# Optimization experiments

Measured on AMD Instinct MI355X. Metric: run time of the kernel, lower is better.

Reference implementation:

```python
import jax, jax.numpy as jnp
import numpy as np

B, N, C, H = 16, 1024, 768, 12
HD = C // H
SCALE = HD ** -0.5


def setup_inputs() -> dict:
    key = jax.random.key(0)
    k1, k2, k3 = jax.random.split(key, 3)
    x = jax.random.normal(k1, (B, N, C), dtype=jnp.float32)
    W_qkv = jax.random.normal(k2, (C, 3 * C), dtype=jnp.float32) * (C ** -0.5)
    W_proj = jax.random.normal(k3, (C, C), dtype=jnp.float32) * (C ** -0.5)
    b_proj = jnp.zeros((C,), dtype=jnp.float32)
    return {"x": x, "W_qkv": W_qkv, "W_proj": W_proj, "b_proj": b_proj}


def reference(x, W_qkv, W_proj, b_proj):
    # qkv projection: [B, N, 3C] -> chunk into q, k, v
    qkv = x @ W_qkv
    q, k, v = jnp.split(qkv, 3, axis=-1)
    # reshape to [B, H, N, HD]
    q = q.reshape(B, N, H, HD).transpose(0, 2, 1, 3)
    k = k.reshape(B, N, H, HD).transpose(0, 2, 1, 3)
    v = v.reshape(B, N, H, HD).transpose(0, 2, 1, 3)
    # manual attention: scores, softmax, weighted sum
    attn = jnp.einsum("bhqd,bhkd->bhqk", q, k) * SCALE
    attn = jax.nn.softmax(attn, axis=-1)
    out = jnp.einsum("bhqk,bhkd->bhqd", attn, v)
    out = out.transpose(0, 2, 1, 3).reshape(B, N, C)
    # output projection
    return out @ W_proj + b_proj
```

## Files before the change

### kernel.cpp

```cpp
#include <hip/hip_runtime.h>

#define B_   16
#define NH   12
#define SEQ  1024
#define CD   768
#define HD_  64
#define MTOT (B_ * SEQ)
#define QSCALE 0.18033688f

typedef __attribute__((ext_vector_type(4)))  float  f32x4;
typedef __attribute__((ext_vector_type(16))) float  f32x16;
typedef __attribute__((ext_vector_type(8)))  __bf16 bf16x8;
typedef __attribute__((ext_vector_type(2)))  unsigned u32x2;

#define WAITV4  asm volatile("s_waitcnt vmcnt(4)" ::: "memory")
#define WAITV0  asm volatile("s_waitcnt vmcnt(0)" ::: "memory")
#define LGKM0   asm volatile("s_waitcnt lgkmcnt(0)" ::: "memory")
#define BAR     __builtin_amdgcn_s_barrier()
#define SB0     __builtin_amdgcn_sched_barrier(0)

__device__ __forceinline__ unsigned short f2bf(float f) {
  unsigned u = __float_as_uint(f);
  u = (u + 0x7FFFu + ((u >> 16) & 1u)) >> 16;
  return (unsigned short)u;
}

__device__ __forceinline__ void gload16(const void* g, void* l) {
  __builtin_amdgcn_global_load_lds(
      (const __attribute__((address_space(1))) void*)g,
      (__attribute__((address_space(3))) void*)l, 16, 0, 0);
}

__device__ __forceinline__ u32x2 pswap(unsigned x, unsigned y) {
  return __builtin_amdgcn_permlane32_swap(x, y, false, false);
}


__global__ __launch_bounds__(256)
void prep_kernel(const float* __restrict__ x,
                 const float* __restrict__ Wqkv,
                 const float* __restrict__ Wproj,
                 unsigned short* __restrict__ xb,
                 unsigned short* __restrict__ wqT,
                 unsigned short* __restrict__ wpT) {
  __shared__ float tile[32][33];
  const int bid = blockIdx.x;
  const int tid = threadIdx.x;
  if (bid < 12288) {
    const int i = bid * 256 + tid;
    float4 f = reinterpret_cast<const float4*>(x)[i];
    uint2 o;
    o.x = (unsigned)f2bf(f.x) | ((unsigned)f2bf(f.y) << 16);
    o.y = (unsigned)f2bf(f.z) | ((unsigned)f2bf(f.w) << 16);
    reinterpret_cast<uint2*>(xb)[i] = o;
  } else {
    const float* W;
    unsigned short* Wt;
    int N, b2;
    if (bid < 12288 + 1728) { b2 = bid - 12288; W = Wqkv; Wt = wqT; N = 2304; }
    else                    { b2 = bid - 14016; W = Wproj; Wt = wpT; N = 768; }
    const int nb = N / 32;
    const int j0 = (b2 % nb) * 32, k0 = (b2 / nb) * 32;
    const int tx = tid & 31, ty = tid >> 5;
    #pragma unroll
    for (int i = 0; i < 4; i++)
      tile[ty + 8 * i][tx] = W[(size_t)(k0 + ty + 8 * i) * N + j0 + tx];
    __syncthreads();
    #pragma unroll
    for (int i = 0; i < 4; i++)
      Wt[(size_t)(j0 + ty + 8 * i) * 768 + k0 + tx] = f2bf(tile[tx][ty + 8 * i]);
  }
}


__device__ __forceinline__ bf16x8 ldsA64(const unsigned short* buf, int row, int g) {
  int byte = (row << 6) + ((g << 4) ^ (((row >> 1) & 3) << 4));
  return *reinterpret_cast<const bf16x8*>((const char*)buf + byte);
}
__device__ __forceinline__ bf16x8 lds128(const unsigned short* buf, int row, int cb) {
  int byte = (row << 7) + (cb ^ ((row & 7) << 4));
  return *reinterpret_cast<const bf16x8*>((const char*)buf + byte);
}


template <int MODE>
__global__ __launch_bounds__(256, 3)
void gemm128_kernel(const unsigned short* __restrict__ A,
                    const unsigned short* __restrict__ Bt,
                    unsigned short* __restrict__ qkvOut,
                    unsigned short* __restrict__ vtOut,
                    float* __restrict__ outF,
                    const float* __restrict__ bias) {
  constexpr int K = 768;
  __shared__ unsigned short sbuf[24576];
  unsigned short* const A0 = sbuf;
  unsigned short* const Bb0 = sbuf + 4096;
  unsigned short* const A1 = sbuf + 8192;
  unsigned short* const Bb1 = sbuf + 12288;
  unsigned short* const A2 = sbuf + 16384;
  unsigned short* const Bb2 = sbuf + 20480;

  const int tid = threadIdx.x;
  const int lane = tid & 63;
  const int wave = tid >> 6;
  const int wm = (wave >> 1) << 6;
  const int wn = (wave & 1) << 6;
  const int m0 = blockIdx.x << 7;
  const int j0 = blockIdx.y << 7;

  const int sr = tid >> 2;
  const int sc = (tid & 3) << 4;
  const int scs = sc ^ (((sr >> 1) & 3) << 4);

  f32x4 acc[4][4] = {};

  const char* const ab  = (const char*)(A  + (size_t)(m0 + sr) * K) + scs;
  const char* const ab2 = (const char*)(A  + (size_t)(m0 + sr + 64) * K) + scs;
  const char* const bb  = (const char*)(Bt + (size_t)(j0 + sr) * K) + scs;
  const char* const bb2 = (const char*)(Bt + (size_t)(j0 + sr + 64) * K) + scs;

  auto stageT = [&](int kt, unsigned short* Ad, unsigned short* Bd) {
    const int kb = kt * 64;
    gload16(ab  + kb, (char*)Ad + tid * 16);
    gload16(ab2 + kb, (char*)Ad + 4096 + tid * 16);
    gload16(bb  + kb, (char*)Bd + tid * 16);
    gload16(bb2 + kb, (char*)Bd + 4096 + tid * 16);
  };

  auto computeT = [&](const unsigned short* As, const unsigned short* Bs) {
    bf16x8 af[4], bf[4];
    const int g = lane >> 4;
    #pragma unroll
    for (int fr = 0; fr < 4; fr++) af[fr] = ldsA64(As, wm + fr * 16 + (lane & 15), g);
    #pragma unroll
    for (int fn = 0; fn < 4; fn++) bf[fn] = ldsA64(Bs, wn + fn * 16 + (lane & 15), g);
    __builtin_amdgcn_s_setprio(1);
    #pragma unroll
    for (int fr = 0; fr < 4; fr++)
      #pragma unroll
      for (int fn = 0; fn < 4; fn++)
        acc[fr][fn] = __builtin_amdgcn_mfma_f32_16x16x32_bf16(af[fr], bf[fn],
                                                              acc[fr][fn], 0, 0, 0);
    __builtin_amdgcn_s_setprio(0);
  };

  stageT(0, A0, Bb0);
  stageT(1, A1, Bb1);

  #pragma unroll 1
  for (int t = 0; t < 21; t += 3) {
    WAITV4; BAR; SB0;
    stageT(t + 2, A2, Bb2);
    computeT(A0, Bb0);

    WAITV4; BAR; SB0;
    stageT(t + 3, A0, Bb0);
    computeT(A1, Bb1);

    WAITV4; BAR; SB0;
    stageT(t + 4, A1, Bb1);
    computeT(A2, Bb2);
  }
  WAITV4; BAR; SB0;
  stageT(23, A2, Bb2);
  computeT(A0, Bb0);
  WAITV4; BAR; SB0;
  computeT(A1, Bb1);
  WAITV0; BAR; SB0;
  computeT(A2, Bb2);

  const int g4 = (lane >> 4) << 2;

  if (MODE == 0) {
    LGKM0; BAR;
    const bool secV = (j0 >= 1536);
    const float scale = (j0 < 768) ? QSCALE : 1.0f;
    char* const ct = (char*)sbuf;
    #pragma unroll
    for (int fr = 0; fr < 4; fr++) {
      #pragma unroll
      for (int fn = 0; fn < 4; fn++) {
        const int j_l = wn + fn * 16 + (lane & 15);
        const int m_l = wm + fr * 16 + g4;
        #pragma unroll
        for (int r = 0; r < 4; r++) {
          const unsigned short v = f2bf(acc[fr][fn][r] * scale);
          const int addr = secV ? (j_l * 288 + (m_l + r) * 2)
                                : ((m_l + r) * 288 + j_l * 2);
          *reinterpret_cast<unsigned short*>(ct + addr) = v;
        }
      }
    }
    LGKM0; BAR;
    const int c = tid & 15, r0 = tid >> 4;
    if (!secV) {
      char* const gb = (char*)qkvOut + (size_t)m0 * 4608 + j0 * 2 + c * 16;
      #pragma unroll
      for (int k = 0; k < 8; k++) {
        const int row = r0 + 16 * k;
        const uint4 d = *reinterpret_cast<const uint4*>(ct + row * 288 + c * 16);
        *reinterpret_cast<uint4*>(gb + (size_t)row * 4608) = d;
      }
    } else {
      const int b = m0 >> 10, nblk = (m0 & 1023) >> 7;
      const int h0 = (j0 - 1536) >> 6;
      char* const vb = (char*)vtOut +
          ((size_t)(b * NH + h0) * 65536 + (size_t)nblk * 8192) * 2 + c * 16;
      #pragma unroll
      for (int k = 0; k < 8; k++) {
        const int row = r0 + 16 * k;
        const uint4 d = *reinterpret_cast<const uint4*>(ct + row * 288 + c * 16);
        const size_t off = ((size_t)(row >> 6) * 65536 + (size_t)(row & 63) * 128) * 2;
        *reinterpret_cast<uint4*>(vb + off) = d;
      }
    }
  } else {
    #pragma unroll
    for (int fr = 0; fr < 4; fr++) {
      #pragma unroll
      for (int fn = 0; fn < 4; fn++) {
        const int jl = j0 + wn + fn * 16 + (lane & 15);
        const int mb = m0 + wm + fr * 16 + g4;
        const float bv = bias[jl];
        #pragma unroll
        for (int r = 0; r < 4; r++)
          outF[(size_t)(mb + r) * CD + jl] = acc[fr][fn][r] + bv;
      }
    }
  }
}


__global__ __launch_bounds__(256, 4)
void attn_kernel(const unsigned short* __restrict__ qkvB,
                 const unsigned short* __restrict__ Vt,
                 unsigned short* __restrict__ Og) {
  __shared__ unsigned short ldsbuf[16384];
  __shared__ float sStat[2][4][32];

  unsigned short* const K0 = ldsbuf;
  unsigned short* const V0 = ldsbuf + 4096;
  unsigned short* const K1 = ldsbuf + 8192;
  unsigned short* const V1 = ldsbuf + 12288;
  unsigned short* const Qs = ldsbuf + 8192;

  const int tid = threadIdx.x;
  const int lane = tid & 63;
  const int wave = tid >> 6;
  const int half = lane >> 5;
  const int q_l = lane & 31;
  const int bh = blockIdx.x;
  const int q0 = blockIdx.y * 128;
  const int b = bh / NH, head = bh - b * NH;

  const int sr = tid >> 3;
  const int scs = ((tid & 7) << 4) ^ ((sr & 7) << 4);

  const char* const xb_ = (const char*)qkvB + (size_t)b * 1024 * 4608;
  const int qoff = head * 128;
  const int koff = qoff + 1536;
  const char* const vb0 = (const char*)Vt + (size_t)bh * 131072;

  {
    #pragma unroll
    for (int i = 0; i < 4; i++)
      gload16(xb_ + (size_t)(q0 + sr + 32 * i) * 4608 + qoff + scs,
              (char*)Qs + (tid + 256 * i) * 16);
    gload16(xb_ + (size_t)sr * 4608 + koff + scs, (char*)K0 + tid * 16);
    gload16(xb_ + (size_t)(sr + 32) * 4608 + koff + scs, (char*)K0 + 4096 + tid * 16);
    gload16(vb0 + sr * 256 + scs, (char*)V0 + tid * 16);
    gload16(vb0 + (sr + 32) * 256 + scs, (char*)V0 + 4096 + tid * 16);
  }
  __syncthreads();

  bf16x8 qf[4];
  #pragma unroll
  for (int c = 0; c < 4; c++)
    qf[c] = lds128(Qs, wave * 32 + q_l, 32 * c + 16 * half);
  __syncthreads();

  f32x16 o0 = {}, o1 = {};
  float mrun = -1e30f, lrun = 0.f;

  for (int t = 0; t < 16; t++) {
    const unsigned short* const Kc = (t & 1) ? K1 : K0;
    const unsigned short* const Vc = (t & 1) ? V1 : V0;
    unsigned short* const Kn = (t & 1) ? K0 : K1;
    unsigned short* const Vn = (t & 1) ? V0 : V1;
    if (t < 15) {
      const int kv1 = (t + 1) * 64;
      const char* const vtile = vb0 + (kv1 >> 7) * 16384 + ((kv1 >> 6) & 1) * 128;
      gload16(xb_ + (size_t)(kv1 + sr) * 4608 + koff + scs, (char*)Kn + tid * 16);
      gload16(xb_ + (size_t)(kv1 + sr + 32) * 4608 + koff + scs,
              (char*)Kn + 4096 + tid * 16);
      gload16(vtile + sr * 256 + scs, (char*)Vn + tid * 16);
      gload16(vtile + (sr + 32) * 256 + scs, (char*)Vn + 4096 + tid * 16);
    }

    f32x16 s0 = {}, s1 = {};
    #pragma unroll
    for (int c = 0; c < 4; c++) {
      bf16x8 kf0 = lds128(Kc, q_l, 32 * c + 16 * half);
      bf16x8 kf1 = lds128(Kc, 32 + q_l, 32 * c + 16 * half);
      s0 = __builtin_amdgcn_mfma_f32_32x32x16_bf16(kf0, qf[c], s0, 0, 0, 0);
      s1 = __builtin_amdgcn_mfma_f32_32x32x16_bf16(kf1, qf[c], s1, 0, 0, 0);
    }

    float vmax = fmaxf(s0[0], s1[0]);
    #pragma unroll
    for (int r = 1; r < 16; r++) vmax = fmaxf(vmax, fmaxf(s0[r], s1[r]));
    {
      u32x2 mx = pswap(__float_as_uint(vmax), __float_as_uint(vmax));
      vmax = fmaxf(__uint_as_float(mx[0]), __uint_as_float(mx[1]));
    }

    if (!__all(vmax <= mrun + 8.0f)) {
      const float mnew = fmaxf(mrun, vmax);
      const float corr = __builtin_amdgcn_exp2f(mrun - mnew);
      mrun = mnew;
      lrun *= corr;
      if (lane < 32) sStat[0][wave][q_l] = corr;
      f32x4 c4[4];
      #pragma unroll
      for (int j = 0; j < 4; j++)
        c4[j] = *reinterpret_cast<const f32x4*>(&sStat[0][wave][4 * half + 8 * j]);
      #pragma unroll
      for (int r = 0; r < 16; r++) {
        const float cc = c4[r >> 2][r & 3];
        o0[r] *= cc;
        o1[r] *= cc;
      }
    }

    float tsum = 0.f;
    #pragma unroll
    for (int r = 0; r < 16; r++) {
      const float p0 = __builtin_amdgcn_exp2f(s0[r] - mrun);
      const float p1 = __builtin_amdgcn_exp2f(s1[r] - mrun);
      s0[r] = p0; s1[r] = p1;
      tsum += p0 + p1;
    }
    {
      u32x2 ts = pswap(__float_as_uint(tsum), __float_as_uint(tsum));
      tsum = __uint_as_float(ts[0]) + __uint_as_float(ts[1]);
    }
    lrun += tsum;

    unsigned pk[2][8];
    #pragma unroll
    for (int w = 0; w < 8; w++) {
      asm("v_cvt_pk_bf16_f32 %0, %1, %2"
          : "=v"(pk[0][w]) : "v"(s0[2 * w]), "v"(s0[2 * w + 1]));
      asm("v_cvt_pk_bf16_f32 %0, %1, %2"
          : "=v"(pk[1][w]) : "v"(s1[2 * w]), "v"(s1[2 * w + 1]));
    }

    #pragma unroll
    for (int c = 0; c < 4; c++) {
      const int st = c >> 1, cc = c & 1;
      u32x2 rA = pswap(pk[st][4 * cc + 0], pk[st][4 * cc + 2]);
      u32x2 rB = pswap(pk[st][4 * cc + 1], pk[st][4 * cc + 3]);
      union { unsigned u[4]; bf16x8 v; } pa;
      pa.u[0] = rA[0]; pa.u[1] = rB[0]; pa.u[2] = rA[1]; pa.u[3] = rB[1];
      bf16x8 vf0 = lds128(Vc, q_l, 32 * c + 16 * half);
      bf16x8 vf1 = lds128(Vc, 32 + q_l, 32 * c + 16 * half);
      o0 = __builtin_amdgcn_mfma_f32_32x32x16_bf16(pa.v, vf0, o0, 0, 0, 0);
      o1 = __builtin_amdgcn_mfma_f32_32x32x16_bf16(pa.v, vf1, o1, 0, 0, 0);
    }
    __syncthreads();
  }

  if (lane < 32) sStat[1][wave][q_l] = lrun;
  f32x4 rl4[4];
  #pragma unroll
  for (int j = 0; j < 4; j++) {
    f32x4 lv = *reinterpret_cast<const f32x4*>(&sStat[1][wave][4 * half + 8 * j]);
    #pragma unroll
    for (int e = 0; e < 4; e++) rl4[j][e] = __builtin_amdgcn_rcpf(lv[e]);
  }
  #pragma unroll
  for (int r = 0; r < 16; r++) {
    const int qq = q0 + wave * 32 + (r & 3) + 8 * (r >> 2) + 4 * half;
    const float rl = rl4[r >> 2][r & 3];
    const size_t base = ((size_t)b * SEQ + qq) * CD + head * HD_;
    Og[base + q_l]      = f2bf(o0[r] * rl);
    Og[base + 32 + q_l] = f2bf(o1[r] * rl);
  }
}


extern "C" void kernel_launch(void* const* d_in, const int* in_sizes, int n_in,
                              void* d_out, int out_size, void* d_ws, size_t ws_size,
                              hipStream_t stream) {
  const float* x     = (const float*)d_in[0];
  const float* Wqkv  = (const float*)d_in[1];
  const float* Wproj = (const float*)d_in[2];
  const float* bproj = (const float*)d_in[3];

  char* ws = (char*)d_ws;
  unsigned short* qkvB = (unsigned short*)(ws + 0);
  unsigned short* Vt   = (unsigned short*)(ws + 75497472);
  unsigned short* xb   = (unsigned short*)(ws + 100663296);
  unsigned short* ao   = (unsigned short*)(ws + 100663296);
  unsigned short* wqT  = (unsigned short*)(ws + 125829120);
  unsigned short* wpT  = (unsigned short*)(ws + 129368064);
  if (ws_size < 130547712ull) return;

  prep_kernel<<<14592, 256, 0, stream>>>(x, Wqkv, Wproj, xb, wqT, wpT);
  gemm128_kernel<0><<<dim3(128, 18), 256, 0, stream>>>(xb, wqT, qkvB, Vt,
                                                       nullptr, nullptr);
  attn_kernel<<<dim3(B_ * NH, SEQ / 128), 256, 0, stream>>>(qkvB, Vt, ao);
  gemm128_kernel<1><<<dim3(128, 6), 256, 0, stream>>>(ao, wpT, nullptr, nullptr,
                                                      (float*)d_out, bproj);
}
```

Before: 195.3 us.

## Split GEMM into QKV and proj kernels with tuned pipelines and coalesced epilogue

Splits the templated GEMM into two specialized kernels. The QKV GEMM moves from triple to double buffering with less LDS and a 296-byte padded transpose stride, so four blocks can fit per CU instead of three. The output projection now stages fp32 accumulators through LDS in two halves and writes bias-added rows as coalesced float4 stores, replacing scattered scalar stores. Double buffering adds an extra barrier per K step, which may expose more load latency.

```diff
diff --git a/kernel.cpp b/kernel.cpp
--- a/kernel.cpp
+++ b/kernel.cpp
@@ -83,14 +83,141 @@
 }
 
 
-template <int MODE>
+__global__ __launch_bounds__(256, 4)
+void gemm_qkv_kernel(const unsigned short* __restrict__ A,
+                     const unsigned short* __restrict__ Bt,
+                     unsigned short* __restrict__ qkvOut,
+                     unsigned short* __restrict__ vtOut) {
+  constexpr int K = 768;
+  __shared__ unsigned short sbuf[18944];
+  unsigned short* const A0 = sbuf;
+  unsigned short* const Bb0 = sbuf + 4096;
+  unsigned short* const A1 = sbuf + 8192;
+  unsigned short* const Bb1 = sbuf + 12288;
+
+  const int tid = threadIdx.x;
+  const int lane = tid & 63;
+  const int wave = tid >> 6;
+  const int wm = (wave >> 1) << 6;
+  const int wn = (wave & 1) << 6;
+  const int m0 = blockIdx.x << 7;
+  const int j0 = blockIdx.y << 7;
+
+  const int sr = tid >> 2;
+  const int sc = (tid & 3) << 4;
+  const int scs = sc ^ (((sr >> 1) & 3) << 4);
+
+  f32x4 acc[4][4] = {};
+
+  const char* const ab  = (const char*)(A  + (size_t)(m0 + sr) * K) + scs;
+  const char* const ab2 = (const char*)(A  + (size_t)(m0 + sr + 64) * K) + scs;
+  const char* const bb  = (const char*)(Bt + (size_t)(j0 + sr) * K) + scs;
+  const char* const bb2 = (const char*)(Bt + (size_t)(j0 + sr + 64) * K) + scs;
+
+  auto stageT = [&](int kt, unsigned short* Ad, unsigned short* Bd) {
+    const int kb = kt * 64;
+    gload16(ab  + kb, (char*)Ad + tid * 16);
+    gload16(ab2 + kb, (char*)Ad + 4096 + tid * 16);
+    gload16(bb  + kb, (char*)Bd + tid * 16);
+    gload16(bb2 + kb, (char*)Bd + 4096 + tid * 16);
+  };
+
+  auto computeT = [&](const unsigned short* As, const unsigned short* Bs) {
+    bf16x8 af[4], bf[4];
+    const int g = lane >> 4;
+    #pragma unroll
+    for (int fr = 0; fr < 4; fr++) af[fr] = ldsA64(As, wm + fr * 16 + (lane & 15), g);
+    #pragma unroll
+    for (int fn = 0; fn < 4; fn++) bf[fn] = ldsA64(Bs, wn + fn * 16 + (lane & 15), g);
+    __builtin_amdgcn_s_setprio(1);
+    #pragma unroll
+    for (int fr = 0; fr < 4; fr++)
+      #pragma unroll
+      for (int fn = 0; fn < 4; fn++)
+        acc[fr][fn] = __builtin_amdgcn_mfma_f32_16x16x32_bf16(af[fr], bf[fn],
+                                                              acc[fr][fn], 0, 0, 0);
+    __builtin_amdgcn_s_setprio(0);
+  };
+
+  stageT(0, A0, Bb0);
+  stageT(1, A1, Bb1);
+
+  #pragma unroll 1
+  for (int t = 0; t < 20; t += 2) {
+    WAITV4; BAR; SB0;
+    computeT(A0, Bb0);
+    SB0; LGKM0; BAR;
+    stageT(t + 2, A0, Bb0);
+
+    WAITV4; BAR; SB0;
+    computeT(A1, Bb1);
+    SB0; LGKM0; BAR;
+    stageT(t + 3, A1, Bb1);
+  }
+  WAITV4; BAR; SB0;
+  computeT(A0, Bb0);
+  SB0; LGKM0; BAR;
+  stageT(22, A0, Bb0);
+  WAITV4; BAR; SB0;
+  computeT(A1, Bb1);
+  SB0; LGKM0; BAR;
+  stageT(23, A1, Bb1);
+  WAITV4; BAR; SB0;
+  computeT(A0, Bb0);
+  WAITV0; BAR; SB0;
+  computeT(A1, Bb1);
+
+  const int g4 = (lane >> 4) << 2;
+  LGKM0; BAR;
+  const bool secV = (j0 >= 1536);
+  const float scale = (j0 < 768) ? QSCALE : 1.0f;
+  char* const ct = (char*)sbuf;
+  #pragma unroll
+  for (int fr = 0; fr < 4; fr++) {
+    #pragma unroll
+    for (int fn = 0; fn < 4; fn++) {
+      const int j_l = wn + fn * 16 + (lane & 15);
+      const int m_l = wm + fr * 16 + g4;
+      #pragma unroll
+      for (int r = 0; r < 4; r++) {
+        const unsigned short v = f2bf(acc[fr][fn][r] * scale);
+        const int addr = secV ? (j_l * 296 + (m_l + r) * 2)
+                              : ((m_l + r) * 296 + j_l * 2);
+        *reinterpret_cast<unsigned short*>(ct + addr) = v;
+      }
+    }
+  }
+  LGKM0; BAR;
+  const int c = tid & 15, r0 = tid >> 4;
+  if (!secV) {
+    char* const gb = (char*)qkvOut + (size_t)m0 * 4608 + j0 * 2 + c * 16;
+    #pragma unroll
+    for (int k = 0; k < 8; k++) {
+      const int row = r0 + 16 * k;
+      const uint4 d = *reinterpret_cast<const uint4*>(ct + row * 296 + c * 16);
+      *reinterpret_cast<uint4*>(gb + (size_t)row * 4608) = d;
+    }
+  } else {
+    const int b = m0 >> 10, nblk = (m0 & 1023) >> 7;
+    const int h0 = (j0 - 1536) >> 6;
+    char* const vb = (char*)vtOut +
+        ((size_t)(b * NH + h0) * 65536 + (size_t)nblk * 8192) * 2 + c * 16;
+    #pragma unroll
+    for (int k = 0; k < 8; k++) {
+      const int row = r0 + 16 * k;
+      const uint4 d = *reinterpret_cast<const uint4*>(ct + row * 296 + c * 16);
+      const size_t off = ((size_t)(row >> 6) * 65536 + (size_t)(row & 63) * 128) * 2;
+      *reinterpret_cast<uint4*>(vb + off) = d;
+    }
+  }
+}
+
+
 __global__ __launch_bounds__(256, 3)
-void gemm128_kernel(const unsigned short* __restrict__ A,
-                    const unsigned short* __restrict__ Bt,
-                    unsigned short* __restrict__ qkvOut,
-                    unsigned short* __restrict__ vtOut,
-                    float* __restrict__ outF,
-                    const float* __restrict__ bias) {
+void gemm_proj_kernel(const unsigned short* __restrict__ A,
+                      const unsigned short* __restrict__ Bt,
+                      float* __restrict__ outF,
+                      const float* __restrict__ bias) {
   constexpr int K = 768;
   __shared__ unsigned short sbuf[24576];
   unsigned short* const A0 = sbuf;
@@ -170,62 +297,31 @@
   computeT(A2, Bb2);
 
   const int g4 = (lane >> 4) << 2;
-
-  if (MODE == 0) {
+  float* const ctf = (float*)sbuf;
+  const int c = tid & 31, rb = tid >> 5;
+  const float4 bv4 = *reinterpret_cast<const float4*>(bias + j0 + c * 4);
+  #pragma unroll
+  for (int p = 0; p < 2; p++) {
     LGKM0; BAR;
-    const bool secV = (j0 >= 1536);
-    const float scale = (j0 < 768) ? QSCALE : 1.0f;
-    char* const ct = (char*)sbuf;
-    #pragma unroll
-    for (int fr = 0; fr < 4; fr++) {
+    if ((wave >> 1) == p) {
       #pragma unroll
-      for (int fn = 0; fn < 4; fn++) {
-        const int j_l = wn + fn * 16 + (lane & 15);
-        const int m_l = wm + fr * 16 + g4;
+      for (int fr = 0; fr < 4; fr++)
         #pragma unroll
-        for (int r = 0; r < 4; r++) {
-          const unsigned short v = f2bf(acc[fr][fn][r] * scale);
-          const int addr = secV ? (j_l * 288 + (m_l + r) * 2)
-                                : ((m_l + r) * 288 + j_l * 2);
-          *reinterpret_cast<unsigned short*>(ct + addr) = v;
+        for (int fn = 0; fn < 4; fn++) {
+          const int col = wn + fn * 16 + (lane & 15);
+          const int lr = fr * 16 + g4;
+          #pragma unroll
+          for (int r = 0; r < 4; r++)
+            ctf[(lr + r) * 132 + col] = acc[fr][fn][r];
         }
-      }
     }
     LGKM0; BAR;
-    const int c = tid & 15, r0 = tid >> 4;
-    if (!secV) {
-      char* const gb = (char*)qkvOut + (size_t)m0 * 4608 + j0 * 2 + c * 16;
-      #pragma unroll
-      for (int k = 0; k < 8; k++) {
-        const int row = r0 + 16 * k;
-        const uint4 d = *reinterpret_cast<const uint4*>(ct + row * 288 + c * 16);
-        *reinterpret_cast<uint4*>(gb + (size_t)row * 4608) = d;
-      }
-    } else {
-      const int b = m0 >> 10, nblk = (m0 & 1023) >> 7;
-      const int h0 = (j0 - 1536) >> 6;
-      char* const vb = (char*)vtOut +
-          ((size_t)(b * NH + h0) * 65536 + (size_t)nblk * 8192) * 2 + c * 16;
-      #pragma unroll
-      for (int k = 0; k < 8; k++) {
-        const int row = r0 + 16 * k;
-        const uint4 d = *reinterpret_cast<const uint4*>(ct + row * 288 + c * 16);
-        const size_t off = ((size_t)(row >> 6) * 65536 + (size_t)(row & 63) * 128) * 2;
-        *reinterpret_cast<uint4*>(vb + off) = d;
-      }
-    }
-  } else {
-    #pragma unroll
-    for (int fr = 0; fr < 4; fr++) {
-      #pragma unroll
-      for (int fn = 0; fn < 4; fn++) {
-        const int jl = j0 + wn + fn * 16 + (lane & 15);
-        const int mb = m0 + wm + fr * 16 + g4;
-        const float bv = bias[jl];
-        #pragma unroll
-        for (int r = 0; r < 4; r++)
-          outF[(size_t)(mb + r) * CD + jl] = acc[fr][fn][r] + bv;
-      }
+    #pragma unroll
+    for (int k = 0; k < 8; k++) {
+      const int row = rb + 8 * k;
+      f32x4 v = *reinterpret_cast<const f32x4*>(&ctf[row * 132 + c * 4]);
+      v[0] += bv4.x; v[1] += bv4.y; v[2] += bv4.z; v[3] += bv4.w;
+      *reinterpret_cast<f32x4*>(outF + (size_t)(m0 + p * 64 + row) * CD + j0 + c * 4) = v;
     }
   }
 }
@@ -407,9 +503,7 @@
   if (ws_size < 130547712ull) return;
 
   prep_kernel<<<14592, 256, 0, stream>>>(x, Wqkv, Wproj, xb, wqT, wpT);
-  gemm128_kernel<0><<<dim3(128, 18), 256, 0, stream>>>(xb, wqT, qkvB, Vt,
-                                                       nullptr, nullptr);
+  gemm_qkv_kernel<<<dim3(128, 18), 256, 0, stream>>>(xb, wqT, qkvB, Vt);
   attn_kernel<<<dim3(B_ * NH, SEQ / 128), 256, 0, stream>>>(qkvB, Vt, ao);
-  gemm128_kernel<1><<<dim3(128, 6), 256, 0, stream>>>(ao, wpT, nullptr, nullptr,
-                                                      (float*)d_out, bproj);
-}
+  gemm_proj_kernel<<<dim3(128, 6), 256, 0, stream>>>(ao, wpT, (float*)d_out, bproj);
+}
```

Measured after the change: 198.4 us. About the same (+1.6%).

## Replace 128x128 GEMM with 256x256 tile, 8-wave, K=128 double-buffered pipeline

Applied to the files above, without the earlier changes.

Rewrites both projection GEMMs to use 256x256 output tiles with 512 threads (8 waves), K-steps of 128, and a double-buffered LDS schedule that interleaves half-tile loads with four MFMA quadrants. The goal is more operand reuse per byte loaded and fewer global loads per FLOP. The output-projection epilogue now goes through LDS for coalesced float4 stores with bias. The grids become small: 576 blocks for QKV and only 192 for the output projection, which can leave many of the 256 CUs idle. The 128 KB LDS footprint also limits occupancy.

```diff
diff --git a/kernel.cpp b/kernel.cpp
--- a/kernel.cpp
+++ b/kernel.cpp
@@ -73,158 +73,204 @@
 }
 
 
-__device__ __forceinline__ bf16x8 ldsA64(const unsigned short* buf, int row, int g) {
-  int byte = (row << 6) + ((g << 4) ^ (((row >> 1) & 3) << 4));
-  return *reinterpret_cast<const bf16x8*>((const char*)buf + byte);
-}
 __device__ __forceinline__ bf16x8 lds128(const unsigned short* buf, int row, int cb) {
   int byte = (row << 7) + (cb ^ ((row & 7) << 4));
   return *reinterpret_cast<const bf16x8*>((const char*)buf + byte);
 }
 
 
+#define READ_AF(FRH)                                                          \
+  _Pragma("unroll") for (int kk = 0; kk < 2; kk++)                            \
+  _Pragma("unroll") for (int i = 0; i < 4; i++)                               \
+    af[kk][i] = lds128(Ac, wm * 128 + (FRH) * 64 + i * 16 + rl, kk * 64 + fcb);
+#define READ_BF(FNH)                                                          \
+  _Pragma("unroll") for (int kk = 0; kk < 2; kk++)                            \
+  _Pragma("unroll") for (int j = 0; j < 2; j++)                               \
+    bf[kk][(FNH) * 2 + j] =                                                   \
+        lds128(Bc, wn * 64 + (FNH) * 32 + j * 16 + rl, kk * 64 + fcb);
+#define MFMA16(FRH, FNH)                                                      \
+  __builtin_amdgcn_s_setprio(1);                                              \
+  _Pragma("unroll") for (int kk = 0; kk < 2; kk++)                            \
+  _Pragma("unroll") for (int i = 0; i < 4; i++)                               \
+  _Pragma("unroll") for (int j = 0; j < 2; j++)                               \
+    acc[(FRH) * 4 + i][(FNH) * 2 + j] = __builtin_amdgcn_mfma_f32_16x16x32_bf16( \
+        af[kk][i], bf[kk][(FNH) * 2 + j], acc[(FRH) * 4 + i][(FNH) * 2 + j],  \
+        0, 0, 0);                                                             \
+  __builtin_amdgcn_s_setprio(0);
+
 template <int MODE>
-__global__ __launch_bounds__(256, 3)
-void gemm128_kernel(const unsigned short* __restrict__ A,
+__global__ __launch_bounds__(512, 2)
+void gemm256_kernel(const unsigned short* __restrict__ A,
                     const unsigned short* __restrict__ Bt,
                     unsigned short* __restrict__ qkvOut,
                     unsigned short* __restrict__ vtOut,
                     float* __restrict__ outF,
                     const float* __restrict__ bias) {
-  constexpr int K = 768;
-  __shared__ unsigned short sbuf[24576];
-  unsigned short* const A0 = sbuf;
-  unsigned short* const Bb0 = sbuf + 4096;
-  unsigned short* const A1 = sbuf + 8192;
-  unsigned short* const Bb1 = sbuf + 12288;
-  unsigned short* const A2 = sbuf + 16384;
-  unsigned short* const Bb2 = sbuf + 20480;
+  __shared__ unsigned short lds[65536];
 
   const int tid = threadIdx.x;
   const int lane = tid & 63;
   const int wave = tid >> 6;
-  const int wm = (wave >> 1) << 6;
-  const int wn = (wave & 1) << 6;
-  const int m0 = blockIdx.x << 7;
-  const int j0 = blockIdx.y << 7;
-
-  const int sr = tid >> 2;
-  const int sc = (tid & 3) << 4;
-  const int scs = sc ^ (((sr >> 1) & 3) << 4);
-
-  f32x4 acc[4][4] = {};
-
-  const char* const ab  = (const char*)(A  + (size_t)(m0 + sr) * K) + scs;
-  const char* const ab2 = (const char*)(A  + (size_t)(m0 + sr + 64) * K) + scs;
-  const char* const bb  = (const char*)(Bt + (size_t)(j0 + sr) * K) + scs;
-  const char* const bb2 = (const char*)(Bt + (size_t)(j0 + sr + 64) * K) + scs;
-
-  auto stageT = [&](int kt, unsigned short* Ad, unsigned short* Bd) {
-    const int kb = kt * 64;
-    gload16(ab  + kb, (char*)Ad + tid * 16);
-    gload16(ab2 + kb, (char*)Ad + 4096 + tid * 16);
-    gload16(bb  + kb, (char*)Bd + tid * 16);
-    gload16(bb2 + kb, (char*)Bd + 4096 + tid * 16);
+  const int wm = wave >> 2;
+  const int wn = wave & 3;
+  const int m0 = blockIdx.x << 8;
+  const int j0 = blockIdx.y << 8;
+  const int rl = lane & 15;
+  const int fcb = (lane >> 4) << 4;
+
+  const int srow = tid >> 3;
+  const int sc16 = (tid & 7) << 4;
+  const int scs = sc16 ^ ((srow & 7) << 4);
+
+  const char* const aRow = (const char*)A  + ((size_t)(m0 + srow) * 768) * 2 + scs;
+  const char* const bRow = (const char*)Bt + ((size_t)(j0 + srow) * 768) * 2 + scs;
+  char* const dRowA = (char*)lds + srow * 128 + sc16;
+
+  f32x4 acc[8][4] = {};
+
+  auto stageA = [&](int kt, int h, int bb) {
+    const char* src = aRow + (size_t)h * 196608 + kt * 128;
+    char* dst = dRowA + bb * 65536 + h * 16384;
+    gload16(src, dst);
+    gload16(src + 98304, dst + 8192);
   };
-
-  auto computeT = [&](const unsigned short* As, const unsigned short* Bs) {
-    bf16x8 af[4], bf[4];
-    const int g = lane >> 4;
-    #pragma unroll
-    for (int fr = 0; fr < 4; fr++) af[fr] = ldsA64(As, wm + fr * 16 + (lane & 15), g);
-    #pragma unroll
-    for (int fn = 0; fn < 4; fn++) bf[fn] = ldsA64(Bs, wn + fn * 16 + (lane & 15), g);
-    __builtin_amdgcn_s_setprio(1);
-    #pragma unroll
-    for (int fr = 0; fr < 4; fr++)
-      #pragma unroll
-      for (int fn = 0; fn < 4; fn++)
-        acc[fr][fn] = __builtin_amdgcn_mfma_f32_16x16x32_bf16(af[fr], bf[fn],
-                                                              acc[fr][fn], 0, 0, 0);
-    __builtin_amdgcn_s_setprio(0);
+  auto stageB = [&](int kt, int h, int bb) {
+    const char* src = bRow + (size_t)h * 196608 + kt * 128;
+    char* dst = dRowA + 32768 + bb * 65536 + h * 16384;
+    gload16(src, dst);
+    gload16(src + 98304, dst + 8192);
   };
 
-  stageT(0, A0, Bb0);
-  stageT(1, A1, Bb1);
+  stageA(0, 0, 0); stageA(0, 1, 0);
+  stageB(0, 0, 0); stageB(0, 1, 0);
+  stageA(1, 0, 1); stageA(1, 1, 1);
+  WAITV4; BAR; SB0;
+
+  bf16x8 af[2][4], bf[2][4];
 
   #pragma unroll 1
-  for (int t = 0; t < 21; t += 3) {
-    WAITV4; BAR; SB0;
-    stageT(t + 2, A2, Bb2);
-    computeT(A0, Bb0);
-
-    WAITV4; BAR; SB0;
-    stageT(t + 3, A0, Bb0);
-    computeT(A1, Bb1);
-
-    WAITV4; BAR; SB0;
-    stageT(t + 4, A1, Bb1);
-    computeT(A2, Bb2);
-  }
-  WAITV4; BAR; SB0;
-  stageT(23, A2, Bb2);
-  computeT(A0, Bb0);
-  WAITV4; BAR; SB0;
-  computeT(A1, Bb1);
-  WAITV0; BAR; SB0;
-  computeT(A2, Bb2);
+  for (int t = 0; t < 12; ++t) {
+    const unsigned short* Ac = lds + (t & 1) * 32768;
+    const unsigned short* Bc = Ac + 16384;
+    const int n = (t & 1) ^ 1;
+    READ_AF(0); READ_BF(0);
+    if (t <= 10) stageB(t + 1, 0, n);
+    BAR; LGKM0; SB0;
+    MFMA16(0, 0);
+    BAR;
+    READ_BF(1);
+    if (t <= 10) stageB(t + 1, 1, n);
+    BAR; LGKM0; SB0;
+    MFMA16(0, 1);
+    BAR;
+    READ_AF(1);
+    if (t <= 9) stageA(t + 2, 0, t & 1);
+    BAR; LGKM0; SB0;
+    MFMA16(1, 1);
+    BAR;
+    if (t <= 9) stageA(t + 2, 1, t & 1);
+    BAR; SB0;
+    MFMA16(1, 0);
+    if (t <= 9) { WAITV4; }
+    else if (t == 10) { WAITV0; }
+    BAR; SB0;
+  }
 
   const int g4 = (lane >> 4) << 2;
 
   if (MODE == 0) {
-    LGKM0; BAR;
     const bool secV = (j0 >= 1536);
     const float scale = (j0 < 768) ? QSCALE : 1.0f;
-    char* const ct = (char*)sbuf;
-    #pragma unroll
-    for (int fr = 0; fr < 4; fr++) {
+    char* const ct = (char*)lds;
+    if (!secV) {
       #pragma unroll
-      for (int fn = 0; fn < 4; fn++) {
-        const int j_l = wn + fn * 16 + (lane & 15);
-        const int m_l = wm + fr * 16 + g4;
+      for (int p = 0; p < 2; p++) {
+        BAR;
+        if (wm == p) {
+          #pragma unroll
+          for (int fr = 0; fr < 8; fr++)
+            #pragma unroll
+            for (int fn = 0; fn < 4; fn++) {
+              const int j_l = wn * 64 + fn * 16 + rl;
+              const int mrow = fr * 16 + g4;
+              #pragma unroll
+              for (int r = 0; r < 4; r++)
+                *reinterpret_cast<unsigned short*>(ct + (mrow + r) * 528 + j_l * 2) =
+                    f2bf(acc[fr][fn][r] * scale);
+            }
+        }
+        LGKM0; BAR;
+        const int c = tid & 31, r0 = tid >> 5;
+        char* const gb = (char*)qkvOut + (size_t)(m0 + p * 128) * 4608 + j0 * 2 + c * 16;
         #pragma unroll
-        for (int r = 0; r < 4; r++) {
-          const unsigned short v = f2bf(acc[fr][fn][r] * scale);
-          const int addr = secV ? (j_l * 288 + (m_l + r) * 2)
-                                : ((m_l + r) * 288 + j_l * 2);
-          *reinterpret_cast<unsigned short*>(ct + addr) = v;
+        for (int k = 0; k < 8; k++) {
+          const int row = r0 + 16 * k;
+          const uint4 d = *reinterpret_cast<const uint4*>(ct + row * 528 + c * 16);
+          *reinterpret_cast<uint4*>(gb + (size_t)row * 4608) = d;
         }
       }
-    }
-    LGKM0; BAR;
-    const int c = tid & 15, r0 = tid >> 4;
-    if (!secV) {
-      char* const gb = (char*)qkvOut + (size_t)m0 * 4608 + j0 * 2 + c * 16;
+    } else {
+      const int bidx = m0 >> 10;
+      const int h0 = (j0 - 1536) >> 6;
+      #pragma unroll
+      for (int p = 0; p < 2; p++) {
+        BAR;
+        if (wm == p) {
+          #pragma unroll
+          for (int fr = 0; fr < 8; fr++)
+            #pragma unroll
+            for (int fn = 0; fn < 4; fn++) {
+              const int j_l = wn * 64 + fn * 16 + rl;
+              const int mrow = fr * 16 + g4;
+              uint2 pkd;
+              pkd.x = (unsigned)f2bf(acc[fr][fn][0]) |
+                      ((unsigned)f2bf(acc[fr][fn][1]) << 16);
+              pkd.y = (unsigned)f2bf(acc[fr][fn][2]) |
+                      ((unsigned)f2bf(acc[fr][fn][3]) << 16);
+              *reinterpret_cast<uint2*>(ct + j_l * 264 + mrow * 2) = pkd;
+            }
+        }
+        LGKM0; BAR;
+        const int c = tid & 15, r0 = tid >> 4;
+        const int nblk = ((m0 & 1023) >> 7) + p;
+        #pragma unroll
+        for (int k = 0; k < 8; k++) {
+          const int jr = r0 + 32 * k;
+          const int h = h0 + (jr >> 6);
+          const int d = jr & 63;
+          const size_t dst = (((size_t)(bidx * NH + h) * 8 + nblk) * 64 + d) * 256 + c * 16;
+          const uint4 v = *reinterpret_cast<const uint4*>(ct + jr * 264 + c * 16);
+          *reinterpret_cast<uint4*>((char*)vtOut + dst) = v;
+        }
+      }
+    }
+  } else {
+    float* const ctf = (float*)lds;
+    const int c = tid & 63, r0 = tid >> 6;
+    float4 bv4 = *reinterpret_cast<const float4*>(bias + j0 + c * 4);
+    #pragma unroll
+    for (int p = 0; p < 4; p++) {
+      BAR;
+      if (wm == (p >> 1)) {
+        #pragma unroll
+        for (int i = 0; i < 4; i++) {
+          const int fr = (p & 1) * 4 + i;
+          #pragma unroll
+          for (int fn = 0; fn < 4; fn++) {
+            const int col = wn * 64 + fn * 16 + rl;
+            #pragma unroll
+            for (int r = 0; r < 4; r++)
+              ctf[(i * 16 + g4 + r) * 260 + col] = acc[fr][fn][r];
+          }
+        }
+      }
+      LGKM0; BAR;
       #pragma unroll
       for (int k = 0; k < 8; k++) {
-        const int row = r0 + 16 * k;
-        const uint4 d = *reinterpret_cast<const uint4*>(ct + row * 288 + c * 16);
-        *reinterpret_cast<uint4*>(gb + (size_t)row * 4608) = d;
-      }
-    } else {
-      const int b = m0 >> 10, nblk = (m0 & 1023) >> 7;
-      const int h0 = (j0 - 1536) >> 6;
-      char* const vb = (char*)vtOut +
-          ((size_t)(b * NH + h0) * 65536 + (size_t)nblk * 8192) * 2 + c * 16;
-      #pragma unroll
-      for (int k = 0; k < 8; k++) {
-        const int row = r0 + 16 * k;
-        const uint4 d = *reinterpret_cast<const uint4*>(ct + row * 288 + c * 16);
-        const size_t off = ((size_t)(row >> 6) * 65536 + (size_t)(row & 63) * 128) * 2;
-        *reinterpret_cast<uint4*>(vb + off) = d;
-      }
-    }
-  } else {
-    #pragma unroll
-    for (int fr = 0; fr < 4; fr++) {
-      #pragma unroll
-      for (int fn = 0; fn < 4; fn++) {
-        const int jl = j0 + wn + fn * 16 + (lane & 15);
-        const int mb = m0 + wm + fr * 16 + g4;
-        const float bv = bias[jl];
-        #pragma unroll
-        for (int r = 0; r < 4; r++)
-          outF[(size_t)(mb + r) * CD + jl] = acc[fr][fn][r] + bv;
+        const int row = r0 + 8 * k;
+        f32x4 v = *reinterpret_cast<const f32x4*>(&ctf[row * 260 + c * 4]);
+        v[0] += bv4.x; v[1] += bv4.y; v[2] += bv4.z; v[3] += bv4.w;
+        *reinterpret_cast<f32x4*>(outF + (size_t)(m0 + p * 64 + row) * CD + j0 + c * 4) = v;
       }
     }
   }
@@ -407,9 +453,9 @@
   if (ws_size < 130547712ull) return;
 
   prep_kernel<<<14592, 256, 0, stream>>>(x, Wqkv, Wproj, xb, wqT, wpT);
-  gemm128_kernel<0><<<dim3(128, 18), 256, 0, stream>>>(xb, wqT, qkvB, Vt,
-                                                       nullptr, nullptr);
+  gemm256_kernel<0><<<dim3(64, 9), 512, 0, stream>>>(xb, wqT, qkvB, Vt,
+                                                     nullptr, nullptr);
   attn_kernel<<<dim3(B_ * NH, SEQ / 128), 256, 0, stream>>>(qkvB, Vt, ao);
-  gemm128_kernel<1><<<dim3(128, 6), 256, 0, stream>>>(ao, wpT, nullptr, nullptr,
-                                                      (float*)d_out, bproj);
-}
+  gemm256_kernel<1><<<dim3(64, 3), 512, 0, stream>>>(ao, wpT, nullptr, nullptr,
+                                                     (float*)d_out, bproj);
+}
```

Result: slower. 304.2 us (+55.8%).
